# Optimization experiments

Hardware: AMD Instinct MI355X
Metric: run time of the kernel (lower is better)

Reference implementation:

```python
import jax, jax.numpy as jnp
import numpy as np

N, E = 40000, 640000
IN, HID, OUT = 128, 128, 128


def _lin(key, fan_in, fan_out):
    bound = 1.0 / np.sqrt(fan_in)
    kw, kb = jax.random.split(key)
    W = jax.random.uniform(kw, (fan_in, fan_out), jnp.float32, -bound, bound)
    b = jax.random.uniform(kb, (fan_out,), jnp.float32, -bound, bound)
    return W, b


def setup_inputs() -> dict:
    key = jax.random.key(0)
    ks = jax.random.split(key, 10)
    node_feat = jax.random.normal(ks[0], (N, IN), jnp.float32)
    coord_feat = jax.random.normal(ks[1], (N, 3), jnp.float32)
    src = jax.random.randint(ks[2], (E,), 0, N, jnp.int32)
    dst = jax.random.randint(ks[3], (E,), 0, N, jnp.int32)
    # edge_mlp: Linear(2*IN+1 -> HID), SiLU, Linear(HID -> HID), SiLU
    We1, be1 = _lin(ks[4], 2 * IN + 1, HID)
    We2, be2 = _lin(ks[5], HID, HID)
    # node_mlp: Linear(IN+HID -> HID), SiLU, Linear(HID -> OUT)
    Wn1, bn1 = _lin(ks[6], IN + HID, HID)
    Wn2, bn2 = _lin(ks[7], HID, OUT)
    # coord_mlp: Linear(HID -> HID), SiLU, Linear(HID -> 1, bias=False)
    Wc1, bc1 = _lin(ks[8], HID, HID)
    Wc2, _ = _lin(ks[9], HID, 1)
    return {"node_feat": node_feat, "coord_feat": coord_feat, "src": src, "dst": dst,
            "We1": We1, "be1": be1, "We2": We2, "be2": be2,
            "Wn1": Wn1, "bn1": bn1, "Wn2": Wn2, "bn2": bn2,
            "Wc1": Wc1, "bc1": bc1, "Wc2": Wc2}


def reference(node_feat, coord_feat, src, dst,
              We1, be1, We2, be2, Wn1, bn1, Wn2, bn2, Wc1, bc1, Wc2):
    n = node_feat.shape[0]
    # edge gather: u_sub_v gives x_src - x_dst
    x_diff = coord_feat[src] - coord_feat[dst]                       # (E, 3)
    dist = jnp.sqrt(jnp.sum(x_diff * x_diff, axis=-1, keepdims=True))  # (E, 1)
    x_dir = x_diff / (dist + 1e-7)
    f = jnp.concatenate([node_feat[src], node_feat[dst], dist], axis=-1)  # (E, 2*IN+1)
    msg_h = jax.nn.silu(jax.nn.silu(f @ We1 + be1) @ We2 + be2)      # (E, HID)
    coef = jax.nn.silu(msg_h @ Wc1 + bc1) @ Wc2                      # (E, 1)
    msg_x = coef * x_dir                                             # (E, 3)
    # scatter-reduce to destination nodes: sum for h, mean for x
    h_neigh = jax.ops.segment_sum(msg_h, dst, num_segments=n)        # (N, HID)
    cnt = jax.ops.segment_sum(jnp.ones((dst.shape[0], 1), msg_x.dtype), dst, num_segments=n)
    x_neigh = jax.ops.segment_sum(msg_x, dst, num_segments=n) / jnp.maximum(cnt, 1.0)
    h = jax.nn.silu(jnp.concatenate([node_feat, h_neigh], axis=-1) @ Wn1 + bn1) @ Wn2 + bn2
    return h, coord_feat + x_neigh
```

## Files before the change

### kernel.cpp

```cpp
#include <hip/hip_runtime.h>
#include <hip/hip_bf16.h>
#include <math.h>
#include <stdint.h>

#define N_NODES 40000
#define N_EDGES 640000

typedef short short8 __attribute__((ext_vector_type(8)));
typedef float f32x4 __attribute__((ext_vector_type(4)));

__device__ __forceinline__ float silu(float x) {
    return __fdividef(x, 1.0f + __expf(-x));
}

__device__ __forceinline__ unsigned short f2bf(float f) {
    unsigned u = __float_as_uint(f);
    u += 0x7FFF + ((u >> 16) & 1);
    return (unsigned short)(u >> 16);
}
__device__ __forceinline__ float bf2f(unsigned short h) {
    return __uint_as_float(((unsigned)h) << 16);
}
__device__ __forceinline__ unsigned pk2bf(float a, float b) {
    __hip_bfloat162 h = __float22bfloat162_rn(make_float2(a, b));
    unsigned u;
    __builtin_memcpy(&u, &h, 4);
    return u;
}

__global__ __launch_bounds__(1024) void k_scanA(const int* __restrict__ deg,
                                                int* __restrict__ rsl,
                                                int* __restrict__ btot) {
    __shared__ int wsum[16];
    const int t = threadIdx.x;
    const int lane = t & 63, wid = t >> 6;
    const int base = blockIdx.x * 1000;
    const int x0 = (t < 1000) ? deg[base + t] : 0;
    int x = x0;
#pragma unroll
    for (int s = 1; s < 64; s <<= 1) {
        const int u = __shfl_up(x, s, 64);
        if (lane >= s) x += u;
    }
    if (lane == 63) wsum[wid] = x;
    __syncthreads();
    if (wid == 0) {
        int ws = (lane < 16) ? wsum[lane] : 0;
#pragma unroll
        for (int s = 1; s < 16; s <<= 1) {
            const int u = __shfl_up(ws, s, 64);
            if (lane >= s) ws += u;
        }
        if (lane < 16) wsum[lane] = ws;
    }
    __syncthreads();
    const int wbase = (wid > 0) ? wsum[wid - 1] : 0;
    if (t < 1000) rsl[base + t] = wbase + x - x0;
    if (t == 0) btot[blockIdx.x] = wsum[15];
}

__global__ __launch_bounds__(64) void k_scanB(const int* __restrict__ btot,
                                              int* __restrict__ bo) {
    const int t = threadIdx.x;
    const int x0 = (t < 40) ? btot[t] : 0;
    int x = x0;
#pragma unroll
    for (int s = 1; s < 64; s <<= 1) {
        const int u = __shfl_up(x, s, 64);
        if (t >= s) x += u;
    }
    if (t < 40) bo[t] = x - x0;
}

__global__ __launch_bounds__(256) void k_fill(const int* __restrict__ dst,
                                              const int* __restrict__ rsl,
                                              const int* __restrict__ bo,
                                              int* __restrict__ cursor,
                                              int* __restrict__ elist) {
    const int e = blockIdx.x * 256 + threadIdx.x;
    if (e < N_EDGES) {
        const int d = dst[e];
        const int p = atomicAdd(&cursor[d], 1);
        elist[bo[d / 1000] + rsl[d] + p] = e;
    }
}

__global__ __launch_bounds__(128) void k_pack2(
    const float* __restrict__ We1, const float* __restrict__ We2,
    const float* __restrict__ Wc1, const float* __restrict__ Wn1,
    const float* __restrict__ Wn2,
    unsigned short* __restrict__ Wt_e1, unsigned short* __restrict__ Wt_e2,
    unsigned short* __restrict__ Wt_c1, unsigned short* __restrict__ Wt_n1,
    unsigned short* __restrict__ Wt_n2,
    int* __restrict__ deg, int* __restrict__ cursor, float* __restrict__ xs,
    float* __restrict__ hn) {
    const int b = blockIdx.x;
    const int t = threadIdx.x;
    Wt_e1[b * 128 + t] = f2bf(We1[(size_t)((b >> 7) * 128 + t) * 128 + (b & 127)]);
    if (b < 128) {
        Wt_e2[b * 128 + t] = f2bf(We2[(size_t)t * 128 + b]);
        Wt_c1[b * 128 + t] = f2bf(Wc1[(size_t)t * 128 + b]);
        Wt_n2[b * 128 + t] = f2bf(Wn2[(size_t)t * 128 + b]);
        Wt_n1[b * 256 + t] = f2bf(Wn1[(size_t)t * 128 + b]);
        Wt_n1[b * 256 + 128 + t] = f2bf(Wn1[(size_t)(128 + t) * 128 + b]);
    }
    const int gid = b * 128 + t;
    for (int i = gid; i < N_NODES; i += 32768) { deg[i] = 0; cursor[i] = 0; }
    for (int i = gid; i < N_NODES * 4; i += 32768) xs[i] = 0.0f;
    float4* hz = (float4*)hn;
    const float4 z4 = {0.f, 0.f, 0.f, 0.f};
    for (int i = gid; i < N_NODES * 32; i += 32768) hz[i] = z4;
}

__global__ __launch_bounds__(256) void k_cntpre(
    const float* __restrict__ nf, const unsigned short* __restrict__ Wt_e1,
    const float* __restrict__ be1,
    unsigned short* __restrict__ Pc,
    const int* __restrict__ dst, int* __restrict__ deg) {
    __shared__ __align__(16) unsigned short sNF[32][136];
    const int t = threadIdx.x;
    const int node0 = blockIdx.x * 32;
    {
        const int e0 = (blockIdx.x * 256 + t) * 2;
        const int d0 = dst[e0], d1 = dst[e0 + 1];
        atomicAdd(&deg[d0], 1);
        atomicAdd(&deg[d1], 1);
    }
    {
        const int m = t >> 3, kc = (t & 7) * 16;
        const float* sp = &nf[(size_t)(node0 + m) * 128 + kc];
        const float4 v0 = *(const float4*)(sp + 0);
        const float4 v1 = *(const float4*)(sp + 4);
        const float4 v2 = *(const float4*)(sp + 8);
        const float4 v3 = *(const float4*)(sp + 12);
        int4 o0, o1;
        o0.x = pk2bf(v0.x, v0.y); o0.y = pk2bf(v0.z, v0.w);
        o0.z = pk2bf(v1.x, v1.y); o0.w = pk2bf(v1.z, v1.w);
        o1.x = pk2bf(v2.x, v2.y); o1.y = pk2bf(v2.z, v2.w);
        o1.z = pk2bf(v3.x, v3.y); o1.w = pk2bf(v3.z, v3.w);
        *(int4*)&sNF[m][kc] = o0;
        *(int4*)&sNF[m][kc + 8] = o1;
    }
    __syncthreads();

    const int w = t >> 6, l = t & 63, c = l & 15, quad = l >> 4;
    const int n0 = w * 64;

    f32x4 acc[2][4];
#pragma unroll
    for (int mt = 0; mt < 2; mt++)
#pragma unroll
        for (int tl = 0; tl < 4; tl++) acc[mt][tl] = (f32x4){0.f, 0.f, 0.f, 0.f};

#pragma unroll
    for (int k0 = 0; k0 < 128; k0 += 32) {
        const short8 a0 = *(const short8*)&sNF[c][k0 + quad * 8];
        const short8 a1 = *(const short8*)&sNF[16 + c][k0 + quad * 8];
#pragma unroll
        for (int tl = 0; tl < 4; tl++) {
            const short8 b = *(const short8*)(Wt_e1 +
                ((size_t)(n0 + tl * 16 + c) << 7) + k0 + quad * 8);
            acc[0][tl] = __builtin_amdgcn_mfma_f32_16x16x32_bf16(a0, b, acc[0][tl], 0, 0, 0);
            acc[1][tl] = __builtin_amdgcn_mfma_f32_16x16x32_bf16(a1, b, acc[1][tl], 0, 0, 0);
        }
    }
#pragma unroll
    for (int mt = 0; mt < 2; mt++)
#pragma unroll
        for (int tl = 0; tl < 4; tl++) {
            const int col = n0 + tl * 16 + c;
            const float bias = (col >= 128) ? be1[col - 128] : 0.0f;
            const unsigned p01 = pk2bf(acc[mt][tl][0] + bias, acc[mt][tl][1] + bias);
            const unsigned p23 = pk2bf(acc[mt][tl][2] + bias, acc[mt][tl][3] + bias);
            const int row = node0 + mt * 16 + quad * 4;
            Pc[(size_t)(row + 0) * 256 + col] = (unsigned short)p01;
            Pc[(size_t)(row + 1) * 256 + col] = (unsigned short)(p01 >> 16);
            Pc[(size_t)(row + 2) * 256 + col] = (unsigned short)p23;
            Pc[(size_t)(row + 3) * 256 + col] = (unsigned short)(p23 >> 16);
        }
}

__global__ __launch_bounds__(256) void k_edge8(
    const unsigned short* __restrict__ Pc, const float* __restrict__ coord,
    const int* __restrict__ src, const int* __restrict__ dst,
    const int* __restrict__ elist,
    const float* __restrict__ We1,
    const unsigned short* __restrict__ Wt_e2, const float* __restrict__ be2,
    const unsigned short* __restrict__ Wt_c1, const float* __restrict__ bc1,
    const float* __restrict__ Wc2,
    float* __restrict__ h_neigh, float* __restrict__ xs) {
    __shared__ __align__(16) unsigned short sT[64][136];
    __shared__ float scoefp[4][32];
    __shared__ float sw[128];
    __shared__ float sdist[64];
    __shared__ float sxd[64][3];
    __shared__ int ssrc[64];
    __shared__ int sdst[64];

    const int t = threadIdx.x;
    const int bid = (int)blockIdx.x;
    const int swz = (bid & 7) * 1250 + (bid >> 3);
    const int e0 = swz * 64;

    if (t < 64) {
        const int eid = elist[e0 + t];
        const int s = src[eid], d = dst[eid];
        ssrc[t] = s; sdst[t] = d;
        const float dx = coord[3 * s + 0] - coord[3 * d + 0];
        const float dy = coord[3 * s + 1] - coord[3 * d + 1];
        const float dz = coord[3 * s + 2] - coord[3 * d + 2];
        const float dist = sqrtf(dx * dx + dy * dy + dz * dz);
        sdist[t] = dist;
        const float inv = __fdividef(1.0f, dist + 1e-7f);
        sxd[t][0] = dx * inv; sxd[t][1] = dy * inv; sxd[t][2] = dz * inv;
    } else if (t < 96) {
        ((float4*)sw)[t - 64] = ((const float4*)(We1 + 256 * 128))[t - 64];
    }
    __syncthreads();

    {
        const int e = t >> 2;
        const int kc = (t & 3) * 32;
        const int s = ssrc[e], d = sdst[e];
        const float dist = sdist[e];
        const unsigned short* p1 = Pc + (size_t)s * 256 + kc;
        const unsigned short* p2 = Pc + (size_t)d * 256 + 128 + kc;
        short8 a[4], b[4];
#pragma unroll
        for (int i = 0; i < 4; i++) {
            a[i] = *(const short8*)(p1 + i * 8);
            b[i] = *(const short8*)(p2 + i * 8);
        }
#pragma unroll
        for (int i = 0; i < 4; i++) {
            float v[8];
#pragma unroll
            for (int kk = 0; kk < 8; kk++) {
                const int k = kc + i * 8 + kk;
                v[kk] = silu(bf2f((unsigned short)a[i][kk]) + bf2f((unsigned short)b[i][kk])
                             + dist * sw[k]);
            }
            int4 o;
            o.x = pk2bf(v[0], v[1]); o.y = pk2bf(v[2], v[3]);
            o.z = pk2bf(v[4], v[5]); o.w = pk2bf(v[6], v[7]);
            *(int4*)&sT[e][kc + i * 8] = o;
        }
    }
    __syncthreads();

    const int w = t >> 6;
    const int l = t & 63;
    const int h = w & 1;
    const int H = w >> 1;
    const int m0 = h * 32;
    const int n0 = H * 64;
    const int c = l & 15;
    const int quad = l >> 4;

    f32x4 acc1[2][4];
#pragma unroll
    for (int mt = 0; mt < 2; mt++)
#pragma unroll
        for (int tile = 0; tile < 4; tile++) acc1[mt][tile] = (f32x4){0.f, 0.f, 0.f, 0.f};
#pragma unroll
    for (int k0 = 0; k0 < 128; k0 += 32) {
        const short8 a0 = *(const short8*)&sT[m0 + c][k0 + quad * 8];
        const short8 a1 = *(const short8*)&sT[m0 + 16 + c][k0 + quad * 8];
#pragma unroll
        for (int tile = 0; tile < 4; tile++) {
            const short8 b = *(const short8*)(Wt_e2 +
                ((size_t)(n0 + tile * 16 + c) << 7) + k0 + quad * 8);
            acc1[0][tile] = __builtin_amdgcn_mfma_f32_16x16x32_bf16(a0, b, acc1[0][tile], 0, 0, 0);
            acc1[1][tile] = __builtin_amdgcn_mfma_f32_16x16x32_bf16(a1, b, acc1[1][tile], 0, 0, 0);
        }
    }
    __syncthreads();

#pragma unroll
    for (int mt = 0; mt < 2; mt++)
#pragma unroll
        for (int tile = 0; tile < 4; tile++) {
            const int col = n0 + tile * 16 + c;
            const float bb = be2[col];
            const unsigned p01 = pk2bf(silu(acc1[mt][tile][0] + bb), silu(acc1[mt][tile][1] + bb));
            const unsigned p23 = pk2bf(silu(acc1[mt][tile][2] + bb), silu(acc1[mt][tile][3] + bb));
            const int row = m0 + mt * 16 + quad * 4;
            sT[row + 0][col] = (unsigned short)p01;
            sT[row + 1][col] = (unsigned short)(p01 >> 16);
            sT[row + 2][col] = (unsigned short)p23;
            sT[row + 3][col] = (unsigned short)(p23 >> 16);
        }
    __syncthreads();

    {
        const int j = t & 127;
        const int q = t >> 7;
        const int eb = q * 32;
        float acc = bf2f(sT[eb][j]);
        int prev = sdst[eb];
        for (int e2 = eb + 1; e2 < eb + 32; e2++) {
            const int de = sdst[e2];
            if (de != prev) {
                atomicAdd(&h_neigh[(size_t)prev * 128 + j], acc);
                acc = 0.0f;
                prev = de;
            }
            acc += bf2f(sT[e2][j]);
        }
        atomicAdd(&h_neigh[(size_t)prev * 128 + j], acc);
    }

    {
        f32x4 acc[2][4];
#pragma unroll
        for (int mt = 0; mt < 2; mt++)
#pragma unroll
            for (int tile = 0; tile < 4; tile++) acc[mt][tile] = (f32x4){0.f, 0.f, 0.f, 0.f};
#pragma unroll
        for (int k0 = 0; k0 < 128; k0 += 32) {
            const short8 a0 = *(const short8*)&sT[m0 + c][k0 + quad * 8];
            const short8 a1 = *(const short8*)&sT[m0 + 16 + c][k0 + quad * 8];
#pragma unroll
            for (int tile = 0; tile < 4; tile++) {
                const short8 b = *(const short8*)(Wt_c1 +
                    ((size_t)(n0 + tile * 16 + c) << 7) + k0 + quad * 8);
                acc[0][tile] = __builtin_amdgcn_mfma_f32_16x16x32_bf16(a0, b, acc[0][tile], 0, 0, 0);
                acc[1][tile] = __builtin_amdgcn_mfma_f32_16x16x32_bf16(a1, b, acc[1][tile], 0, 0, 0);
            }
        }
        float part[2][4] = {{0.f, 0.f, 0.f, 0.f}, {0.f, 0.f, 0.f, 0.f}};
#pragma unroll
        for (int tile = 0; tile < 4; tile++) {
            const int col = n0 + tile * 16 + c;
            const float bc = bc1[col];
            const float wc = Wc2[col];
#pragma unroll
            for (int mt = 0; mt < 2; mt++)
#pragma unroll
                for (int r = 0; r < 4; r++)
                    part[mt][r] += silu(acc[mt][tile][r] + bc) * wc;
        }
#pragma unroll
        for (int off = 1; off < 16; off <<= 1) {
#pragma unroll
            for (int mt = 0; mt < 2; mt++)
#pragma unroll
                for (int r = 0; r < 4; r++)
                    part[mt][r] += __shfl_xor(part[mt][r], off, 64);
        }
        if (c == 0) {
#pragma unroll
            for (int mt = 0; mt < 2; mt++)
#pragma unroll
                for (int r = 0; r < 4; r++)
                    scoefp[w][mt * 16 + quad * 4 + r] = part[mt][r];
        }
    }

    if (l < 3) {
        const int cc = l;
        const int eb = h * 32;
        float acc = scoefp[w][0] * sxd[eb][cc];
        int prev = sdst[eb];
        for (int e2 = eb + 1; e2 < eb + 32; e2++) {
            const int de = sdst[e2];
            if (de != prev) {
                atomicAdd(&xs[(size_t)prev * 4 + cc], acc);
                acc = 0.0f;
                prev = de;
            }
            acc += scoefp[w][e2 & 31] * sxd[e2][cc];
        }
        atomicAdd(&xs[(size_t)prev * 4 + cc], acc);
    }
}

__global__ __launch_bounds__(256) void k_node(
    const float* __restrict__ nf, const float* __restrict__ coord,
    const float* __restrict__ hn, const float* __restrict__ xs,
    const int* __restrict__ deg,
    const unsigned short* __restrict__ Wt_n1, const float* __restrict__ bn1,
    const unsigned short* __restrict__ Wt_n2, const float* __restrict__ bn2,
    float* __restrict__ out_h, float* __restrict__ out_x) {
    __shared__ __align__(16) unsigned short sAB[32][264];
    __shared__ __align__(16) unsigned short sH[32][136];
    const int t = threadIdx.x;
    const int node0 = blockIdx.x * 32;
    {
        const int m = t >> 3, kc = (t & 7) * 32;
        const float* base = (kc < 128) ? &nf[(size_t)(node0 + m) * 128 + kc]
                                       : &hn[(size_t)(node0 + m) * 128 + (kc - 128)];
#pragma unroll
        for (int kk = 0; kk < 32; kk += 8) {
            const float4 v0 = *(const float4*)(base + kk);
            const float4 v1 = *(const float4*)(base + kk + 4);
            int4 o;
            o.x = pk2bf(v0.x, v0.y); o.y = pk2bf(v0.z, v0.w);
            o.z = pk2bf(v1.x, v1.y); o.w = pk2bf(v1.z, v1.w);
            *(int4*)&sAB[m][kc + kk] = o;
        }
    }
    if (t < 96) {
        const int m = t / 3, cc = t - m * 3;
        const int i = node0 + m;
        const float cnt = (float)deg[i];
        out_x[(size_t)i * 3 + cc] =
            coord[(size_t)i * 3 + cc] + __fdividef(xs[(size_t)i * 4 + cc], fmaxf(cnt, 1.0f));
    }
    __syncthreads();

    const int w = t >> 6, l = t & 63, c = l & 15, quad = l >> 4;
    const int n0 = w * 32;

    {
        f32x4 acc[2][2];
#pragma unroll
        for (int mt = 0; mt < 2; mt++)
#pragma unroll
            for (int tl = 0; tl < 2; tl++) acc[mt][tl] = (f32x4){0.f, 0.f, 0.f, 0.f};
#pragma unroll
        for (int k0 = 0; k0 < 256; k0 += 32) {
            const short8 a0 = *(const short8*)&sAB[c][k0 + quad * 8];
            const short8 a1 = *(const short8*)&sAB[16 + c][k0 + quad * 8];
#pragma unroll
            for (int tl = 0; tl < 2; tl++) {
                const short8 b = *(const short8*)(Wt_n1 +
                    ((size_t)(n0 + tl * 16 + c) << 8) + k0 + quad * 8);
                acc[0][tl] = __builtin_amdgcn_mfma_f32_16x16x32_bf16(a0, b, acc[0][tl], 0, 0, 0);
                acc[1][tl] = __builtin_amdgcn_mfma_f32_16x16x32_bf16(a1, b, acc[1][tl], 0, 0, 0);
            }
        }
#pragma unroll
        for (int mt = 0; mt < 2; mt++)
#pragma unroll
            for (int tl = 0; tl < 2; tl++) {
                const int col = n0 + tl * 16 + c;
                const float bb = bn1[col];
                const unsigned p01 = pk2bf(silu(acc[mt][tl][0] + bb), silu(acc[mt][tl][1] + bb));
                const unsigned p23 = pk2bf(silu(acc[mt][tl][2] + bb), silu(acc[mt][tl][3] + bb));
                const int row = mt * 16 + quad * 4;
                sH[row + 0][col] = (unsigned short)p01;
                sH[row + 1][col] = (unsigned short)(p01 >> 16);
                sH[row + 2][col] = (unsigned short)p23;
                sH[row + 3][col] = (unsigned short)(p23 >> 16);
            }
    }
    __syncthreads();

    {
        f32x4 acc[2][2];
#pragma unroll
        for (int mt = 0; mt < 2; mt++)
#pragma unroll
            for (int tl = 0; tl < 2; tl++) acc[mt][tl] = (f32x4){0.f, 0.f, 0.f, 0.f};
#pragma unroll
        for (int k0 = 0; k0 < 128; k0 += 32) {
            const short8 a0 = *(const short8*)&sH[c][k0 + quad * 8];
            const short8 a1 = *(const short8*)&sH[16 + c][k0 + quad * 8];
#pragma unroll
            for (int tl = 0; tl < 2; tl++) {
                const short8 b = *(const short8*)(Wt_n2 +
                    ((size_t)(n0 + tl * 16 + c) << 7) + k0 + quad * 8);
                acc[0][tl] = __builtin_amdgcn_mfma_f32_16x16x32_bf16(a0, b, acc[0][tl], 0, 0, 0);
                acc[1][tl] = __builtin_amdgcn_mfma_f32_16x16x32_bf16(a1, b, acc[1][tl], 0, 0, 0);
            }
        }
#pragma unroll
        for (int mt = 0; mt < 2; mt++)
#pragma unroll
            for (int tl = 0; tl < 2; tl++) {
                const int col = n0 + tl * 16 + c;
                const float bb = bn2[col];
#pragma unroll
                for (int r = 0; r < 4; r++) {
                    const int row = mt * 16 + quad * 4 + r;
                    out_h[(size_t)(node0 + row) * 128 + col] = acc[mt][tl][r] + bb;
                }
            }
    }
}

extern "C" void kernel_launch(void* const* d_in, const int* in_sizes, int n_in,
                              void* d_out, int out_size, void* d_ws, size_t ws_size,
                              hipStream_t stream) {
    const float* nf    = (const float*)d_in[0];
    const float* coord = (const float*)d_in[1];
    const int*   src   = (const int*)d_in[2];
    const int*   dst   = (const int*)d_in[3];
    const float* We1   = (const float*)d_in[4];
    const float* be1   = (const float*)d_in[5];
    const float* We2   = (const float*)d_in[6];
    const float* be2   = (const float*)d_in[7];
    const float* Wn1   = (const float*)d_in[8];
    const float* bn1   = (const float*)d_in[9];
    const float* Wn2   = (const float*)d_in[10];
    const float* bn2   = (const float*)d_in[11];
    const float* Wc1   = (const float*)d_in[12];
    const float* bc1   = (const float*)d_in[13];
    const float* Wc2   = (const float*)d_in[14];

    unsigned short* Pc = (unsigned short*)d_ws;
    float* hn = (float*)(Pc + (size_t)N_NODES * 256);
    float* xs = hn + (size_t)N_NODES * 128;
    int* deg       = (int*)(xs + (size_t)N_NODES * 4);
    int* rsl       = deg + N_NODES;
    int* cursor    = rsl + N_NODES;
    int* btot      = cursor + N_NODES;
    int* bo        = btot + 64;
    int* elist     = bo + 64;
    unsigned short* Wt_e1 = (unsigned short*)
        (((uintptr_t)(elist + N_EDGES) + 255) & ~(uintptr_t)255);
    unsigned short* Wt_e2 = Wt_e1 + 256 * 128;
    unsigned short* Wt_c1 = Wt_e2 + 128 * 128;
    unsigned short* Wt_n1 = Wt_c1 + 128 * 128;
    unsigned short* Wt_n2 = Wt_n1 + 128 * 256;

    float* out_h = (float*)d_out;
    float* out_x = out_h + (size_t)N_NODES * 128;

    k_pack2<<<256, 128, 0, stream>>>(We1, We2, Wc1, Wn1, Wn2,
                                     Wt_e1, Wt_e2, Wt_c1, Wt_n1, Wt_n2,
                                     deg, cursor, xs, hn);
    k_cntpre<<<N_NODES / 32, 256, 0, stream>>>(nf, Wt_e1, be1, Pc, dst, deg);
    k_scanA<<<40, 1024, 0, stream>>>(deg, rsl, btot);
    k_scanB<<<1, 64, 0, stream>>>(btot, bo);
    k_fill<<<(N_EDGES + 255) / 256, 256, 0, stream>>>(dst, rsl, bo, cursor, elist);
    k_edge8<<<N_EDGES / 64, 256, 0, stream>>>(Pc, coord, src, dst, elist,
                                              We1, Wt_e2, be2, Wt_c1, bc1,
                                              Wc2, hn, xs);
    k_node<<<N_NODES / 32, 256, 0, stream>>>(nf, coord, hn, xs, deg,
                                             Wt_n1, bn1, Wt_n2, bn2, out_h, out_x);
}
```

Before: 426.3 us.

## Fold block-offset scan into fill kernel and parallelize edge segment reductions

```diff
diff --git a/kernel.cpp b/kernel.cpp
--- a/kernel.cpp
+++ b/kernel.cpp
@@ -59,29 +59,29 @@
     if (t == 0) btot[blockIdx.x] = wsum[15];
 }
 
-__global__ __launch_bounds__(64) void k_scanB(const int* __restrict__ btot,
-                                              int* __restrict__ bo) {
-    const int t = threadIdx.x;
-    const int x0 = (t < 40) ? btot[t] : 0;
-    int x = x0;
-#pragma unroll
-    for (int s = 1; s < 64; s <<= 1) {
-        const int u = __shfl_up(x, s, 64);
-        if (t >= s) x += u;
-    }
-    if (t < 40) bo[t] = x - x0;
-}
-
 __global__ __launch_bounds__(256) void k_fill(const int* __restrict__ dst,
                                               const int* __restrict__ rsl,
-                                              const int* __restrict__ bo,
+                                              const int* __restrict__ btot,
                                               int* __restrict__ cursor,
                                               int* __restrict__ elist) {
-    const int e = blockIdx.x * 256 + threadIdx.x;
+    __shared__ int sbo[40];
+    const int t = threadIdx.x;
+    if (t < 64) {
+        const int x0 = (t < 40) ? btot[t] : 0;
+        int x = x0;
+#pragma unroll
+        for (int s = 1; s < 64; s <<= 1) {
+            const int u = __shfl_up(x, s, 64);
+            if (t >= s) x += u;
+        }
+        if (t < 40) sbo[t] = x - x0;
+    }
+    __syncthreads();
+    const int e = blockIdx.x * 256 + t;
     if (e < N_EDGES) {
         const int d = dst[e];
         const int p = atomicAdd(&cursor[d], 1);
-        elist[bo[d / 1000] + rsl[d] + p] = e;
+        elist[sbo[d / 1000] + rsl[d] + p] = e;
     }
 }
 
@@ -180,7 +180,7 @@
         }
 }
 
-__global__ __launch_bounds__(256) void k_edge8(
+__global__ __launch_bounds__(256) void k_edge9(
     const unsigned short* __restrict__ Pc, const float* __restrict__ coord,
     const int* __restrict__ src, const int* __restrict__ dst,
     const int* __restrict__ elist,
@@ -296,18 +296,21 @@
         const int j = t & 127;
         const int q = t >> 7;
         const int eb = q * 32;
-        float acc = bf2f(sT[eb][j]);
-        int prev = sdst[eb];
-        for (int e2 = eb + 1; e2 < eb + 32; e2++) {
-            const int de = sdst[e2];
-            if (de != prev) {
-                atomicAdd(&h_neigh[(size_t)prev * 128 + j], acc);
-                acc = 0.0f;
-                prev = de;
-            }
-            acc += bf2f(sT[e2][j]);
-        }
-        atomicAdd(&h_neigh[(size_t)prev * 128 + j], acc);
+        float aA = bf2f(sT[eb][j]);      int pA = sdst[eb];
+        float aB = bf2f(sT[eb + 16][j]); int pB = sdst[eb + 16];
+#pragma unroll
+        for (int i = 1; i < 16; i++) {
+            const int dA = sdst[eb + i];
+            const int dB = sdst[eb + 16 + i];
+            const float vA = bf2f(sT[eb + i][j]);
+            const float vB = bf2f(sT[eb + 16 + i][j]);
+            if (dA != pA) { atomicAdd(&h_neigh[(size_t)pA * 128 + j], aA); aA = 0.f; pA = dA; }
+            aA += vA;
+            if (dB != pB) { atomicAdd(&h_neigh[(size_t)pB * 128 + j], aB); aB = 0.f; pB = dB; }
+            aB += vB;
+        }
+        atomicAdd(&h_neigh[(size_t)pA * 128 + j], aA);
+        atomicAdd(&h_neigh[(size_t)pB * 128 + j], aB);
     }
 
     {
@@ -357,21 +360,26 @@
         }
     }
 
-    if (l < 3) {
-        const int cc = l;
-        const int eb = h * 32;
-        float acc = scoefp[w][0] * sxd[eb][cc];
-        int prev = sdst[eb];
-        for (int e2 = eb + 1; e2 < eb + 32; e2++) {
-            const int de = sdst[e2];
-            if (de != prev) {
-                atomicAdd(&xs[(size_t)prev * 4 + cc], acc);
-                acc = 0.0f;
-                prev = de;
-            }
-            acc += scoefp[w][e2 & 31] * sxd[e2][cc];
-        }
-        atomicAdd(&xs[(size_t)prev * 4 + cc], acc);
+    if (l < 32) {
+        const int e = h * 32 + l;
+        const int d = sdst[e];
+        const float cf = scoefp[w][l];
+        float v0 = cf * sxd[e][0];
+        float v1 = cf * sxd[e][1];
+        float v2 = cf * sxd[e][2];
+#pragma unroll
+        for (int s = 1; s < 32; s <<= 1) {
+            const float u0 = __shfl_down(v0, s, 64);
+            const float u1 = __shfl_down(v1, s, 64);
+            const float u2 = __shfl_down(v2, s, 64);
+            const int ud = __shfl_down(d, s, 64);
+            if (l + s < 32 && ud == d) { v0 += u0; v1 += u1; v2 += u2; }
+        }
+        if (l == 0 || sdst[e - 1] != d) {
+            atomicAdd(&xs[(size_t)d * 4 + 0], v0);
+            atomicAdd(&xs[(size_t)d * 4 + 1], v1);
+            atomicAdd(&xs[(size_t)d * 4 + 2], v2);
+        }
     }
 }
 
@@ -506,8 +514,7 @@
     int* rsl       = deg + N_NODES;
     int* cursor    = rsl + N_NODES;
     int* btot      = cursor + N_NODES;
-    int* bo        = btot + 64;
-    int* elist     = bo + 64;
+    int* elist     = btot + 64;
     unsigned short* Wt_e1 = (unsigned short*)
         (((uintptr_t)(elist + N_EDGES) + 255) & ~(uintptr_t)255);
     unsigned short* Wt_e2 = Wt_e1 + 256 * 128;
@@ -523,9 +530,8 @@
                                      deg, cursor, xs, hn);
     k_cntpre<<<N_NODES / 32, 256, 0, stream>>>(nf, Wt_e1, be1, Pc, dst, deg);
     k_scanA<<<40, 1024, 0, stream>>>(deg, rsl, btot);
-    k_scanB<<<1, 64, 0, stream>>>(btot, bo);
-    k_fill<<<(N_EDGES + 255) / 256, 256, 0, stream>>>(dst, rsl, bo, cursor, elist);
-    k_edge8<<<N_EDGES / 64, 256, 0, stream>>>(Pc, coord, src, dst, elist,
+    k_fill<<<(N_EDGES + 255) / 256, 256, 0, stream>>>(dst, rsl, btot, cursor, elist);
+    k_edge9<<<N_EDGES / 64, 256, 0, stream>>>(Pc, coord, src, dst, elist,
                                               We1, Wt_e2, be2, Wt_c1, bc1,
                                               Wc2, hn, xs);
     k_node<<<N_NODES / 32, 256, 0, stream>>>(nf, coord, hn, xs, deg,
```

Result: faster. 413.4 us (-3.0%).
